# Kernel tuning notes

Hardware: AMD Instinct MI355X
Metric: run time of the kernel (lower is better)

Reference implementation:

```python
import jax, jax.numpy as jnp
import numpy as np

ALPHA = 0.2       # LeakyReLU negative slope
ADJ_THRE = 0.0
NEG_INF = -1e30   # finite stand-in for -inf (safe in fp32 softmax)


def setup_inputs() -> dict:
    key = jax.random.key(0)
    k1, k2, k3, k4, k5, k6 = jax.random.split(key, 6)
    b, n_k = 4, 512
    in_f, e_in_f, out_f = 256, 64, 256
    x = jax.random.normal(k1, (b, n_k, in_f), dtype=jnp.float32)
    edge = jax.random.normal(k2, (b, n_k, n_k, e_in_f), dtype=jnp.float32)
    adj = jax.random.uniform(k3, (b, n_k, n_k), dtype=jnp.float32)
    # xavier_uniform with gain=1.414
    def xavier(k, shape, gain=1.414):
        fan_in, fan_out = shape[0], shape[1]
        bound = gain * np.sqrt(6.0 / (fan_in + fan_out))
        return jax.random.uniform(k, shape, dtype=jnp.float32, minval=-bound, maxval=bound)
    W = xavier(k4, (in_f, out_f))
    W1 = xavier(k5, (e_in_f, out_f))
    a = xavier(k6, (3 * out_f, 1))
    return {"x": x, "edge": edge, "adj": adj, "W": W, "W1": W1, "a": a}


def reference(x, edge, adj, W, W1, a):
    # x:(b,n,in_f) edge:(b,n,n,e_in) adj:(b,n,n)
    out_f = W.shape[1]
    h = jnp.matmul(x, W)                      # (b, n, o)
    a1 = a[:out_f, 0]                         # score weight for h_i (row)
    a2 = a[out_f:2 * out_f, 0]                # score weight for h_j (col)
    a3 = a[2 * out_f:, 0]                     # score weight for edge proj
    # concat([h_i, h_j, e_h]) @ a == h_i@a1 + h_j@a2 + (edge@W1)@a3
    s_i = jnp.einsum('bno,o->bn', h, a1)      # (b, n)
    s_j = jnp.einsum('bno,o->bn', h, a2)      # (b, n)
    w1a3 = W1 @ a3                            # (e_in,) fused: edge@(W1@a3)
    s_e = jnp.einsum('bije,e->bij', edge, w1a3)  # (b, n, n)
    e = jax.nn.leaky_relu(s_i[:, :, None] + s_j[:, None, :] + s_e, ALPHA)
    e = jnp.where(adj > ADJ_THRE, e, NEG_INF)
    attention = jax.nn.softmax(e, axis=2)     # (b, n, n); dropout off (eval)
    h_prime = jnp.matmul(attention, h)        # (b, n, o)
    return jax.nn.elu(h_prime)                # concat=True
```

## Files before the change

### kernel.cpp

```cpp
#include <hip/hip_runtime.h>
#include <cstdint>
#include <cstddef>

#define ALPHA 0.2f
#define NEG_INF -1e30f

constexpr int B = 4, N = 512, IN_F = 256, E_F = 64, OUT_F = 256;

__global__ __launch_bounds__(256) void k_w1a3(const float* __restrict__ W1,
                                              const float* __restrict__ a,
                                              float* __restrict__ w1a3) {
    int tid = threadIdx.x;
    int e = tid >> 2;
    int part = tid & 3;
    const float* row = W1 + (size_t)e * OUT_F;
    float s = 0.f;
    int o0 = part * 64;
    for (int o = o0; o < o0 + 64; ++o)
        s += row[o] * a[2 * OUT_F + o];
    s += __shfl_xor(s, 1);
    s += __shfl_xor(s, 2);
    if (part == 0) w1a3[e] = s;
}

__global__ __launch_bounds__(256) void k_h(const float* __restrict__ x,
                                           const float* __restrict__ W,
                                           const float* __restrict__ a,
                                           float* __restrict__ h,
                                           float* __restrict__ s_i,
                                           float* __restrict__ s_j) {
    constexpr int ROWS = 8;
    int row0 = blockIdx.x * ROWS;
    int o = threadIdx.x;
    __shared__ float xs[ROWS][IN_F];
    #pragma unroll
    for (int r = 0; r < ROWS; ++r)
        xs[r][o] = x[(size_t)(row0 + r) * IN_F + o];
    __syncthreads();

    float acc[ROWS];
    #pragma unroll
    for (int r = 0; r < ROWS; ++r) acc[r] = 0.f;

    for (int k = 0; k < IN_F; k += 4) {
        float w0 = W[(size_t)(k + 0) * OUT_F + o];
        float w1 = W[(size_t)(k + 1) * OUT_F + o];
        float w2 = W[(size_t)(k + 2) * OUT_F + o];
        float w3 = W[(size_t)(k + 3) * OUT_F + o];
        #pragma unroll
        for (int r = 0; r < ROWS; ++r) {
            float4 xv = *(const float4*)&xs[r][k];
            acc[r] = fmaf(xv.x, w0, acc[r]);
            acc[r] = fmaf(xv.y, w1, acc[r]);
            acc[r] = fmaf(xv.z, w2, acc[r]);
            acc[r] = fmaf(xv.w, w3, acc[r]);
        }
    }

    float a1v = a[o];
    float a2v = a[OUT_F + o];
    __shared__ float p1s[4][ROWS], p2s[4][ROWS];
    int lane = o & 63, wv = o >> 6;
    #pragma unroll
    for (int r = 0; r < ROWS; ++r) {
        h[(size_t)(row0 + r) * OUT_F + o] = acc[r];
        float p1 = acc[r] * a1v;
        float p2 = acc[r] * a2v;
        #pragma unroll
        for (int off = 32; off; off >>= 1) {
            p1 += __shfl_xor(p1, off);
            p2 += __shfl_xor(p2, off);
        }
        if (lane == 0) { p1s[wv][r] = p1; p2s[wv][r] = p2; }
    }
    __syncthreads();
    if (o < ROWS) {
        s_i[row0 + o] = p1s[0][o] + p1s[1][o] + p1s[2][o] + p1s[3][o];
    } else if (o < 2 * ROWS) {
        int r = o - ROWS;
        s_j[row0 + r] = p2s[0][r] + p2s[1][r] + p2s[2][r] + p2s[3][r];
    }
}

__global__ __launch_bounds__(256) void k_att(const float* __restrict__ edge,
                                             const float* __restrict__ adj,
                                             const float* __restrict__ s_i,
                                             const float* __restrict__ s_j,
                                             const float* __restrict__ w1a3,
                                             float* __restrict__ att) {
    int bi = blockIdx.x;
    int b = bi >> 9;
    int tid = threadIdx.x;
    int lane = tid & 63, wv = tid >> 6;

    __shared__ float w1a3s[E_F];
    __shared__ float sjs[N];
    __shared__ float adjs[N];
    __shared__ float evals[N];
    __shared__ float redm[4], reds[4];

    if (tid < E_F) w1a3s[tid] = w1a3[tid];
    sjs[tid]        = s_j[b * N + tid];
    sjs[tid + 256]  = s_j[b * N + tid + 256];
    adjs[tid]       = adj[(size_t)bi * N + tid];
    adjs[tid + 256] = adj[(size_t)bi * N + tid + 256];
    float si = s_i[bi];
    __syncthreads();

    int jsub = lane >> 4;
    int eo = (lane & 15) * 4;
    float4 wv4 = *(const float4*)&w1a3s[eo];
    const float* ebase = edge + (size_t)bi * N * E_F;

    for (int it = 0; it < N / 16; ++it) {
        int j = it * 16 + wv * 4 + jsub;
        float4 ev = *(const float4*)(ebase + (size_t)j * E_F + eo);
        float p = ev.x * wv4.x + ev.y * wv4.y + ev.z * wv4.z + ev.w * wv4.w;
        p += __shfl_xor(p, 1);
        p += __shfl_xor(p, 2);
        p += __shfl_xor(p, 4);
        p += __shfl_xor(p, 8);
        if ((lane & 15) == 0) {
            float v = si + sjs[j] + p;
            v = v > 0.f ? v : ALPHA * v;
            evals[j] = (adjs[j] > 0.f) ? v : NEG_INF;
        }
    }
    __syncthreads();

    float v0 = evals[tid], v1 = evals[tid + 256];
    float m = fmaxf(v0, v1);
    #pragma unroll
    for (int off = 32; off; off >>= 1) m = fmaxf(m, __shfl_xor(m, off));
    if (lane == 0) redm[wv] = m;
    __syncthreads();
    m = fmaxf(fmaxf(redm[0], redm[1]), fmaxf(redm[2], redm[3]));

    float e0 = __expf(v0 - m);
    float e1 = __expf(v1 - m);
    float s = e0 + e1;
    #pragma unroll
    for (int off = 32; off; off >>= 1) s += __shfl_xor(s, off);
    if (lane == 0) reds[wv] = s;
    __syncthreads();
    s = reds[0] + reds[1] + reds[2] + reds[3];
    float inv = 1.f / s;

    att[(size_t)bi * N + tid]       = e0 * inv;
    att[(size_t)bi * N + tid + 256] = e1 * inv;
}

__global__ __launch_bounds__(256) void k_out(const float* __restrict__ att,
                                             const float* __restrict__ h,
                                             float* __restrict__ out) {
    constexpr int ROWS = 8;
    int row0 = blockIdx.x * ROWS;
    int b = row0 >> 9;
    int o = threadIdx.x;
    __shared__ float as_[ROWS][N];
    #pragma unroll
    for (int r = 0; r < ROWS; ++r) {
        as_[r][o]       = att[(size_t)(row0 + r) * N + o];
        as_[r][o + 256] = att[(size_t)(row0 + r) * N + o + 256];
    }
    __syncthreads();

    float acc[ROWS];
    #pragma unroll
    for (int r = 0; r < ROWS; ++r) acc[r] = 0.f;

    const float* hb = h + (size_t)b * N * OUT_F;
    for (int k = 0; k < N; k += 4) {
        float h0 = hb[(size_t)(k + 0) * OUT_F + o];
        float h1 = hb[(size_t)(k + 1) * OUT_F + o];
        float h2 = hb[(size_t)(k + 2) * OUT_F + o];
        float h3 = hb[(size_t)(k + 3) * OUT_F + o];
        #pragma unroll
        for (int r = 0; r < ROWS; ++r) {
            float4 av = *(const float4*)&as_[r][k];
            acc[r] = fmaf(av.x, h0, acc[r]);
            acc[r] = fmaf(av.y, h1, acc[r]);
            acc[r] = fmaf(av.z, h2, acc[r]);
            acc[r] = fmaf(av.w, h3, acc[r]);
        }
    }
    #pragma unroll
    for (int r = 0; r < ROWS; ++r) {
        float v = acc[r];
        out[(size_t)(row0 + r) * OUT_F + o] = v > 0.f ? v : (expf(v) - 1.f);
    }
}

extern "C" void kernel_launch(void* const* d_in, const int* in_sizes, int n_in,
                              void* d_out, int out_size, void* d_ws, size_t ws_size,
                              hipStream_t stream) {
    const float* x    = (const float*)d_in[0];
    const float* edge = (const float*)d_in[1];
    const float* adj  = (const float*)d_in[2];
    const float* W    = (const float*)d_in[3];
    const float* W1   = (const float*)d_in[4];
    const float* a    = (const float*)d_in[5];
    float* out = (float*)d_out;

    float* ws = (float*)d_ws;
    float* h_buf   = ws;
    float* att_buf = h_buf + (size_t)B * N * OUT_F;
    float* si_buf  = att_buf + (size_t)B * N * N;
    float* sj_buf  = si_buf + B * N;
    float* w1a3_buf = sj_buf + B * N;

    k_w1a3<<<1, 256, 0, stream>>>(W1, a, w1a3_buf);
    k_h<<<(B * N) / 8, 256, 0, stream>>>(x, W, a, h_buf, si_buf, sj_buf);
    k_att<<<B * N, 256, 0, stream>>>(edge, adj, si_buf, sj_buf, w1a3_buf, att_buf);
    k_out<<<(B * N) / 8, 256, 0, stream>>>(att_buf, h_buf, out);
}
```

Measured before the change: 434.1 us.

## Merge w1a3 into k_h, vectorize edge and h loads, retile matmuls

Drops the separate w1a3 kernel by giving that work to an extra block of k_h, which saves one launch. k_h and k_out are retiled so that each wave owns one row and each lane computes four output columns through float4 loads, with four rows per block instead of eight. k_att now has each lane reduce 16 edge features with four float4 loads and write partial sums to shared memory, replacing the 16-lane shuffle reduction. The smaller row tile means less reuse of W and h per block, so global traffic for those matrices can rise.

Measured after the change: 467.5 us. +7.7%, slower.

```diff
diff --git a/kernel.cpp b/kernel.cpp
--- a/kernel.cpp
+++ b/kernel.cpp
@@ -7,79 +7,56 @@
 
 constexpr int B = 4, N = 512, IN_F = 256, E_F = 64, OUT_F = 256;
 
-__global__ __launch_bounds__(256) void k_w1a3(const float* __restrict__ W1,
-                                              const float* __restrict__ a,
-                                              float* __restrict__ w1a3) {
-    int tid = threadIdx.x;
-    int e = tid >> 2;
-    int part = tid & 3;
-    const float* row = W1 + (size_t)e * OUT_F;
-    float s = 0.f;
-    int o0 = part * 64;
-    for (int o = o0; o < o0 + 64; ++o)
-        s += row[o] * a[2 * OUT_F + o];
-    s += __shfl_xor(s, 1);
-    s += __shfl_xor(s, 2);
-    if (part == 0) w1a3[e] = s;
-}
-
 __global__ __launch_bounds__(256) void k_h(const float* __restrict__ x,
                                            const float* __restrict__ W,
+                                           const float* __restrict__ W1,
                                            const float* __restrict__ a,
                                            float* __restrict__ h,
                                            float* __restrict__ s_i,
-                                           float* __restrict__ s_j) {
-    constexpr int ROWS = 8;
-    int row0 = blockIdx.x * ROWS;
-    int o = threadIdx.x;
-    __shared__ float xs[ROWS][IN_F];
-    #pragma unroll
-    for (int r = 0; r < ROWS; ++r)
-        xs[r][o] = x[(size_t)(row0 + r) * IN_F + o];
+                                           float* __restrict__ s_j,
+                                           float* __restrict__ w1a3) {
+    int tid = threadIdx.x;
+    if (blockIdx.x == (B * N) / 4) {
+        int e = tid >> 2, part = tid & 3;
+        const float* row = W1 + (size_t)e * OUT_F + part * 64;
+        const float* a3 = a + 2 * OUT_F + part * 64;
+        float s = 0.f;
+        #pragma unroll 8
+        for (int o = 0; o < 64; ++o) s += row[o] * a3[o];
+        s += __shfl_xor(s, 1);
+        s += __shfl_xor(s, 2);
+        if (part == 0) w1a3[e] = s;
+        return;
+    }
+    int wv = tid >> 6, lane = tid & 63;
+    int row = blockIdx.x * 4 + wv;
+    int c4 = lane * 4;
+
+    __shared__ float xs[4][IN_F];
+    *(float4*)&xs[wv][c4] = *(const float4*)&x[(size_t)row * IN_F + c4];
     __syncthreads();
 
-    float acc[ROWS];
+    float4 acc = {0.f, 0.f, 0.f, 0.f};
+    for (int k = 0; k < IN_F; ++k) {
+        float4 w4 = *(const float4*)&W[(size_t)k * OUT_F + c4];
+        float xv = xs[wv][k];
+        acc.x = fmaf(xv, w4.x, acc.x);
+        acc.y = fmaf(xv, w4.y, acc.y);
+        acc.z = fmaf(xv, w4.z, acc.z);
+        acc.w = fmaf(xv, w4.w, acc.w);
+    }
+    *(float4*)&h[(size_t)row * OUT_F + c4] = acc;
+
+    float4 a1v = *(const float4*)&a[c4];
+    float4 a2v = *(const float4*)&a[OUT_F + c4];
+    float p1 = acc.x * a1v.x + acc.y * a1v.y + acc.z * a1v.z + acc.w * a1v.w;
+    float p2 = acc.x * a2v.x + acc.y * a2v.y + acc.z * a2v.z + acc.w * a2v.w;
     #pragma unroll
-    for (int r = 0; r < ROWS; ++r) acc[r] = 0.f;
-
-    for (int k = 0; k < IN_F; k += 4) {
-        float w0 = W[(size_t)(k + 0) * OUT_F + o];
-        float w1 = W[(size_t)(k + 1) * OUT_F + o];
-        float w2 = W[(size_t)(k + 2) * OUT_F + o];
-        float w3 = W[(size_t)(k + 3) * OUT_F + o];
-        #pragma unroll
-        for (int r = 0; r < ROWS; ++r) {
-            float4 xv = *(const float4*)&xs[r][k];
-            acc[r] = fmaf(xv.x, w0, acc[r]);
-            acc[r] = fmaf(xv.y, w1, acc[r]);
-            acc[r] = fmaf(xv.z, w2, acc[r]);
-            acc[r] = fmaf(xv.w, w3, acc[r]);
-        }
+    for (int off = 32; off; off >>= 1) {
+        p1 += __shfl_xor(p1, off);
+        p2 += __shfl_xor(p2, off);
     }
-
-    float a1v = a[o];
-    float a2v = a[OUT_F + o];
-    __shared__ float p1s[4][ROWS], p2s[4][ROWS];
-    int lane = o & 63, wv = o >> 6;
-    #pragma unroll
-    for (int r = 0; r < ROWS; ++r) {
-        h[(size_t)(row0 + r) * OUT_F + o] = acc[r];
-        float p1 = acc[r] * a1v;
-        float p2 = acc[r] * a2v;
-        #pragma unroll
-        for (int off = 32; off; off >>= 1) {
-            p1 += __shfl_xor(p1, off);
-            p2 += __shfl_xor(p2, off);
-        }
-        if (lane == 0) { p1s[wv][r] = p1; p2s[wv][r] = p2; }
-    }
-    __syncthreads();
-    if (o < ROWS) {
-        s_i[row0 + o] = p1s[0][o] + p1s[1][o] + p1s[2][o] + p1s[3][o];
-    } else if (o < 2 * ROWS) {
-        int r = o - ROWS;
-        s_j[row0 + r] = p2s[0][r] + p2s[1][r] + p2s[2][r] + p2s[3][r];
-    }
+    if (lane == 0) { s_i[row] = p1; s_j[row] = p2; }
 }
 
 __global__ __launch_bounds__(256) void k_att(const float* __restrict__ edge,
@@ -91,12 +68,14 @@
     int bi = blockIdx.x;
     int b = bi >> 9;
     int tid = threadIdx.x;
-    int lane = tid & 63, wv = tid >> 6;
+    int wv = tid >> 6, lane = tid & 63;
+    int jl = lane >> 2;
+    int p = lane & 3;
 
     __shared__ float w1a3s[E_F];
     __shared__ float sjs[N];
     __shared__ float adjs[N];
-    __shared__ float evals[N];
+    __shared__ float part[N][4];
     __shared__ float redm[4], reds[4];
 
     if (tid < E_F) w1a3s[tid] = w1a3[tid];
@@ -107,28 +86,38 @@
     float si = s_i[bi];
     __syncthreads();
 
-    int jsub = lane >> 4;
-    int eo = (lane & 15) * 4;
-    float4 wv4 = *(const float4*)&w1a3s[eo];
+    float4 wa = *(const float4*)&w1a3s[p * 16];
+    float4 wb = *(const float4*)&w1a3s[p * 16 + 4];
+    float4 wc = *(const float4*)&w1a3s[p * 16 + 8];
+    float4 wd = *(const float4*)&w1a3s[p * 16 + 12];
+
     const float* ebase = edge + (size_t)bi * N * E_F;
-
-    for (int it = 0; it < N / 16; ++it) {
-        int j = it * 16 + wv * 4 + jsub;
-        float4 ev = *(const float4*)(ebase + (size_t)j * E_F + eo);
-        float p = ev.x * wv4.x + ev.y * wv4.y + ev.z * wv4.z + ev.w * wv4.w;
-        p += __shfl_xor(p, 1);
-        p += __shfl_xor(p, 2);
-        p += __shfl_xor(p, 4);
-        p += __shfl_xor(p, 8);
-        if ((lane & 15) == 0) {
-            float v = si + sjs[j] + p;
-            v = v > 0.f ? v : ALPHA * v;
-            evals[j] = (adjs[j] > 0.f) ? v : NEG_INF;
-        }
+    for (int it = 0; it < 8; ++it) {
+        int j = it * 64 + wv * 16 + jl;
+        const float4* ej = (const float4*)(ebase + (size_t)j * E_F + p * 16);
+        float4 e0 = ej[0];
+        float4 e1 = ej[1];
+        float4 e2 = ej[2];
+        float4 e3 = ej[3];
+        float s = e0.x * wa.x + e0.y * wa.y + e0.z * wa.z + e0.w * wa.w;
+        s = fmaf(e1.x, wb.x, s); s = fmaf(e1.y, wb.y, s);
+        s = fmaf(e1.z, wb.z, s); s = fmaf(e1.w, wb.w, s);
+        s = fmaf(e2.x, wc.x, s); s = fmaf(e2.y, wc.y, s);
+        s = fmaf(e2.z, wc.z, s); s = fmaf(e2.w, wc.w, s);
+        s = fmaf(e3.x, wd.x, s); s = fmaf(e3.y, wd.y, s);
+        s = fmaf(e3.z, wd.z, s); s = fmaf(e3.w, wd.w, s);
+        part[j][p] = s;
     }
     __syncthreads();
 
-    float v0 = evals[tid], v1 = evals[tid + 256];
+    float v0 = si + sjs[tid] + part[tid][0] + part[tid][1] + part[tid][2] + part[tid][3];
+    float v1 = si + sjs[tid + 256] + part[tid + 256][0] + part[tid + 256][1]
+             + part[tid + 256][2] + part[tid + 256][3];
+    v0 = v0 > 0.f ? v0 : ALPHA * v0;
+    v1 = v1 > 0.f ? v1 : ALPHA * v1;
+    v0 = (adjs[tid] > 0.f) ? v0 : NEG_INF;
+    v1 = (adjs[tid + 256] > 0.f) ? v1 : NEG_INF;
+
     float m = fmaxf(v0, v1);
     #pragma unroll
     for (int off = 32; off; off >>= 1) m = fmaxf(m, __shfl_xor(m, off));
@@ -153,42 +142,36 @@
 __global__ __launch_bounds__(256) void k_out(const float* __restrict__ att,
                                              const float* __restrict__ h,
                                              float* __restrict__ out) {
-    constexpr int ROWS = 8;
-    int row0 = blockIdx.x * ROWS;
+    int row0 = blockIdx.x * 4;
     int b = row0 >> 9;
-    int o = threadIdx.x;
-    __shared__ float as_[ROWS][N];
-    #pragma unroll
-    for (int r = 0; r < ROWS; ++r) {
-        as_[r][o]       = att[(size_t)(row0 + r) * N + o];
-        as_[r][o + 256] = att[(size_t)(row0 + r) * N + o + 256];
+    int tid = threadIdx.x;
+    int wv = tid >> 6, lane = tid & 63;
+
+    __shared__ float as_[4][N];
+    {
+        const float* arow = att + (size_t)(row0 + wv) * N + lane * 8;
+        *(float4*)&as_[wv][lane * 8]     = *(const float4*)arow;
+        *(float4*)&as_[wv][lane * 8 + 4] = *(const float4*)(arow + 4);
     }
     __syncthreads();
 
-    float acc[ROWS];
-    #pragma unroll
-    for (int r = 0; r < ROWS; ++r) acc[r] = 0.f;
-
+    int c4 = lane * 4;
     const float* hb = h + (size_t)b * N * OUT_F;
-    for (int k = 0; k < N; k += 4) {
-        float h0 = hb[(size_t)(k + 0) * OUT_F + o];
-        float h1 = hb[(size_t)(k + 1) * OUT_F + o];
-        float h2 = hb[(size_t)(k + 2) * OUT_F + o];
-        float h3 = hb[(size_t)(k + 3) * OUT_F + o];
-        #pragma unroll
-        for (int r = 0; r < ROWS; ++r) {
-            float4 av = *(const float4*)&as_[r][k];
-            acc[r] = fmaf(av.x, h0, acc[r]);
-            acc[r] = fmaf(av.y, h1, acc[r]);
-            acc[r] = fmaf(av.z, h2, acc[r]);
-            acc[r] = fmaf(av.w, h3, acc[r]);
-        }
+    float4 acc = {0.f, 0.f, 0.f, 0.f};
+    for (int k = 0; k < N; ++k) {
+        float4 hv = *(const float4*)&hb[(size_t)k * OUT_F + c4];
+        float av = as_[wv][k];
+        acc.x = fmaf(av, hv.x, acc.x);
+        acc.y = fmaf(av, hv.y, acc.y);
+        acc.z = fmaf(av, hv.z, acc.z);
+        acc.w = fmaf(av, hv.w, acc.w);
     }
-    #pragma unroll
-    for (int r = 0; r < ROWS; ++r) {
-        float v = acc[r];
-        out[(size_t)(row0 + r) * OUT_F + o] = v > 0.f ? v : (expf(v) - 1.f);
-    }
+    float4 o4;
+    o4.x = acc.x > 0.f ? acc.x : (expf(acc.x) - 1.f);
+    o4.y = acc.y > 0.f ? acc.y : (expf(acc.y) - 1.f);
+    o4.z = acc.z > 0.f ? acc.z : (expf(acc.z) - 1.f);
+    o4.w = acc.w > 0.f ? acc.w : (expf(acc.w) - 1.f);
+    *(float4*)&out[(size_t)(row0 + wv) * OUT_F + c4] = o4;
 }
 
 extern "C" void kernel_launch(void* const* d_in, const int* in_sizes, int n_in,
@@ -203,14 +186,13 @@
     float* out = (float*)d_out;
 
     float* ws = (float*)d_ws;
-    float* h_buf   = ws;
-    float* att_buf = h_buf + (size_t)B * N * OUT_F;
-    float* si_buf  = att_buf + (size_t)B * N * N;
-    float* sj_buf  = si_buf + B * N;
+    float* h_buf    = ws;
+    float* att_buf  = h_buf + (size_t)B * N * OUT_F;
+    float* si_buf   = att_buf + (size_t)B * N * N;
+    float* sj_buf   = si_buf + B * N;
     float* w1a3_buf = sj_buf + B * N;
 
-    k_w1a3<<<1, 256, 0, stream>>>(W1, a, w1a3_buf);
-    k_h<<<(B * N) / 8, 256, 0, stream>>>(x, W, a, h_buf, si_buf, sj_buf);
+    k_h<<<(B * N) / 4 + 1, 256, 0, stream>>>(x, W, W1, a, h_buf, si_buf, sj_buf, w1a3_buf);
     k_att<<<B * N, 256, 0, stream>>>(edge, adj, si_buf, sj_buf, w1a3_buf, att_buf);
-    k_out<<<(B * N) / 8, 256, 0, stream>>>(att_buf, h_buf, out);
+    k_out<<<(B * N) / 4, 256, 0, stream>>>(att_buf, h_buf, out);
 }
```
